# Kernel optimization log

Measured on AMD Instinct MI355X. Metric: run time of the kernel, lower is better.

## Reference

```python
import jax, jax.numpy as jnp
import numpy as np

MASK_ID = -100
L, D, HID, NH = 10, 768, 3072, 12
DH = D // NH
REACH = 2  # (sliding_window_size - 1) // 2 with window 5


def _layernorm(x, g, b, eps=1e-5):
    mu = x.mean(-1, keepdims=True)
    var = ((x - mu) ** 2).mean(-1, keepdims=True)
    return (x - mu) * jax.lax.rsqrt(var + eps) * g + b


def _adaln(x, temb, w, bb, g, be):
    # AdaLayerNormShiftScale: linear(silu(temb)) -> (scale, shift)
    e = jax.nn.silu(temb) @ w + bb
    scale, shift = jnp.split(e, 2, axis=-1)
    return _layernorm(x, g, be) * (1.0 + scale) + shift


def _timestep_emb(t):
    half = D // 2
    exponent = -np.log(10000.0) * jnp.arange(half, dtype=jnp.float32) / (half - 1.0)
    freq = jnp.exp(exponent)  # [half]
    emb = t.astype(jnp.float32)[..., None] * freq  # [b,s,half]
    return jnp.concatenate([jnp.sin(emb), jnp.cos(emb)], axis=-1)  # [b,s,D]


def setup_inputs():
    key = jax.random.key(0)
    ks = jax.random.split(key, 16)
    b, s = 4, 1024
    # packed token ids: 4 samples of 256 tokens (16x16 grid), last 64 tokens padding
    idx = np.arange(s)
    sid = idx // 256
    hpos = (idx % 256) // 16
    wpos = idx % 16
    sid = np.where(idx >= 960, MASK_ID, sid)
    tok = np.stack([sid, hpos, wpos], axis=-1)  # [s,3]
    token_ids = jnp.asarray(np.broadcast_to(tok, (b, s, 3)).copy(), dtype=jnp.int32)
    t = jax.random.randint(ks[0], (b, 1), 0, L + 1).astype(jnp.int32)
    t = jnp.broadcast_to(t, (b, s))

    def w(k, shape):
        return jax.random.normal(k, shape, jnp.float32) * 0.02

    return dict(
        x=jax.random.normal(ks[1], (b, s, D), jnp.float32),
        t=t,
        token_ids=token_ids,
        proj_in_w=w(ks[2], (D, D)), proj_in_b=jnp.zeros((D,), jnp.float32),
        h_emb=w(ks[3], (64, D)), w_emb=w(ks[4], (64, D)),
        adaln1_w=w(ks[5], (L, D, 2 * D)), adaln1_b=jnp.zeros((L, 2 * D), jnp.float32),
        ln1_g=jnp.ones((L, D), jnp.float32), ln1_b=jnp.zeros((L, D), jnp.float32),
        qkv_w=w(ks[6], (L, D, 3 * D)), qkv_b=jnp.zeros((L, 3 * D), jnp.float32),
        o_w=w(ks[7], (L, D, D)), o_b=jnp.zeros((L, D), jnp.float32),
        adaln2_w=w(ks[8], (L, D, 2 * D)), adaln2_b=jnp.zeros((L, 2 * D), jnp.float32),
        ln2_g=jnp.ones((L, D), jnp.float32), ln2_b=jnp.zeros((L, D), jnp.float32),
        fc1_w=w(ks[9], (L, D, HID)), fc1_b=jnp.zeros((L, HID), jnp.float32),
        fc2_w=w(ks[10], (L, HID, D)), fc2_b=jnp.zeros((L, D), jnp.float32),
        nout_w=w(ks[11], (D, 2 * D)), nout_b=jnp.zeros((2 * D,), jnp.float32),
        nout_g=jnp.ones((D,), jnp.float32), nout_beta=jnp.zeros((D,), jnp.float32),
    )


def _encoder(x, t, token_ids, proj_in_w, proj_in_b, h_emb, w_emb,
             adaln1_w, adaln1_b, ln1_g, ln1_b, qkv_w, qkv_b, o_w, o_b,
             adaln2_w, adaln2_b, ln2_g, ln2_b, fc1_w, fc1_b, fc2_w, fc2_b,
             nout_w, nout_b, nout_g, nout_beta):
    b, s, _ = x.shape
    sample_ids = token_ids[..., 0]          # [b,s]
    pos = token_ids[..., 1:]                # [b,s,2]
    x = x @ proj_in_w + proj_in_b
    x = x + h_emb[pos[..., 0]] + w_emb[pos[..., 1]]

    # block-sparse mask: same packed sample, Chebyshev sliding window, no padding queries
    same = sample_ids[:, :, None] == sample_ids[:, None, :]              # [b,s,s]
    cheby = jnp.abs(pos[:, :, None, :] - pos[:, None, :, :]).max(-1)      # [b,s,s]
    notpad_q = (sample_ids != MASK_ID)[:, :, None]
    mask = same & (cheby <= REACH) & notpad_q                             # [b,s,s]
    row_valid = mask.any(-1)[..., None]                                   # [b,s,1]

    temb = _timestep_emb(t)  # [b,s,D]
    scale = 1.0 / np.sqrt(DH)
    for i in range(L):
        h1 = _adaln(x, temb, adaln1_w[i], adaln1_b[i], ln1_g[i], ln1_b[i])
        qkv = h1 @ qkv_w[i] + qkv_b[i]
        q, k, v = jnp.split(qkv, 3, axis=-1)
        q = q.reshape(b, s, NH, DH)
        k = k.reshape(b, s, NH, DH)
        v = v.reshape(b, s, NH, DH)
        scores = jnp.einsum('bqhd,bkhd->bhqk', q, k) * scale
        scores = jnp.where(mask[:, None], scores, -1e30)
        attn = jax.nn.softmax(scores, axis=-1)
        o = jnp.einsum('bhqk,bkhd->bqhd', attn, v).reshape(b, s, D)
        o = jnp.where(row_valid, o, 0.0)  # fully-masked (padding) rows -> 0
        x = x + o @ o_w[i] + o_b[i]
        h2 = _adaln(x, temb, adaln2_w[i], adaln2_b[i], ln2_g[i], ln2_b[i])
        x = x + jax.nn.gelu(h2 @ fc1_w[i] + fc1_b[i], approximate=False) @ fc2_w[i] + fc2_b[i]
    x = _adaln(x, temb, nout_w, nout_b, nout_g, nout_beta)
    return x


def reference(x, t, token_ids, proj_in_w, proj_in_b, h_emb, w_emb,
              adaln1_w, adaln1_b, ln1_g, ln1_b, qkv_w, qkv_b, o_w, o_b,
              adaln2_w, adaln2_b, ln2_g, ln2_b, fc1_w, fc1_b, fc2_w, fc2_b,
              nout_w, nout_b, nout_g, nout_beta):
    return _encoder(x, t, token_ids, proj_in_w, proj_in_b, h_emb, w_emb,
                    adaln1_w, adaln1_b, ln1_g, ln1_b, qkv_w, qkv_b, o_w, o_b,
                    adaln2_w, adaln2_b, ln2_g, ln2_b, fc1_w, fc1_b, fc2_w, fc2_b,
                    nout_w, nout_b, nout_g, nout_beta)
```

## Files before the change

### kernel.cpp

```cpp
#include <hip/hip_runtime.h>
#include <hip/hip_bf16.h>
#include <math.h>

#define MASK_ID (-100)
#define SEQ 1024
#define BATCH 4
#define DMODEL 768
#define NHEAD 12
#define DHEAD 64
#define NLAYER 10
#define HIDDEN 3072

typedef unsigned short ushort_t;
typedef unsigned int uint_t;

__device__ __forceinline__ ushort_t f2bf(float f) {
    uint_t u = __float_as_uint(f);
    u = u + 0x7fffu + ((u >> 16) & 1u);
    return (ushort_t)(u >> 16);
}
__device__ __forceinline__ float bf2f(ushort_t u) {
    return __uint_as_float(((uint_t)u) << 16);
}

__device__ __forceinline__ void async_ld16(ushort_t* lds, const ushort_t* g) {
    __builtin_amdgcn_global_load_lds((__attribute__((address_space(1))) const void*)g,
                                     (__attribute__((address_space(3))) void*)lds, 16, 0, 0);
}

__global__ void temb_silu_kernel(const int* __restrict__ t, float* __restrict__ stemb) {
    int b = blockIdx.x;
    int j = threadIdx.x;
    float tv = (float)t[b * SEQ];
    float freq = expf(-logf(10000.f) * (float)j / 383.f);
    float arg = tv * freq;
    float s = sinf(arg), c = cosf(arg);
    stemb[b * DMODEL + j]       = s / (1.f + expf(-s));
    stemb[b * DMODEL + 384 + j] = c / (1.f + expf(-c));
}

__global__ __launch_bounds__(256)
void adaln_partial_kernel(const float* __restrict__ stemb,
                          const float* __restrict__ a1w,
                          const float* __restrict__ a2w,
                          const float* __restrict__ nw,
                          float* __restrict__ partial) {
    int chunk = blockIdx.x;
    int kc    = blockIdx.y;
    int slot  = blockIdx.z;
    int tid = threadIdx.x;
    int col = chunk * 256 + tid;
    const float* W;
    if (slot == 20) W = nw;
    else {
        int i = slot >> 1;
        W = ((slot & 1) ? a2w : a1w) + (size_t)i * DMODEL * 2 * DMODEL;
    }
    __shared__ float sb[4 * 96];
    for (int idx = tid; idx < 4 * 96; idx += 256) {
        int bb = idx / 96, kk = idx % 96;
        sb[idx] = stemb[bb * DMODEL + kc * 96 + kk];
    }
    __syncthreads();
    const float* Wp = W + (size_t)(kc * 96) * (2 * DMODEL) + col;
    float a0 = 0.f, a1 = 0.f, a2 = 0.f, a3 = 0.f;
    #pragma unroll 4
    for (int kk = 0; kk < 96; ++kk) {
        float w = Wp[(size_t)kk * (2 * DMODEL)];
        a0 = fmaf(sb[kk], w, a0);
        a1 = fmaf(sb[96 + kk], w, a1);
        a2 = fmaf(sb[192 + kk], w, a2);
        a3 = fmaf(sb[288 + kk], w, a3);
    }
    size_t base = ((size_t)(slot * 8 + kc) * 4) * (2 * DMODEL) + col;
    partial[base + 0 * 2 * DMODEL] = a0;
    partial[base + 1 * 2 * DMODEL] = a1;
    partial[base + 2 * 2 * DMODEL] = a2;
    partial[base + 3 * 2 * DMODEL] = a3;
}

__global__ __launch_bounds__(256)
void adaln_reduce_kernel(const float* __restrict__ partial,
                         const float* __restrict__ a1b, const float* __restrict__ a2b,
                         const float* __restrict__ nb,
                         float* __restrict__ e_all) {
    int chunk = blockIdx.x;
    int slot  = blockIdx.y;
    int col = chunk * 256 + threadIdx.x;
    const float* bb;
    if (slot == 20) bb = nb;
    else {
        int i = slot >> 1;
        bb = ((slot & 1) ? a2b : a1b) + i * 2 * DMODEL;
    }
    float bias = bb[col];
    float s0 = bias, s1 = bias, s2 = bias, s3 = bias;
    #pragma unroll
    for (int kc = 0; kc < 8; ++kc) {
        size_t base = ((size_t)(slot * 8 + kc) * 4) * (2 * DMODEL) + col;
        s0 += partial[base + 0 * 2 * DMODEL];
        s1 += partial[base + 1 * 2 * DMODEL];
        s2 += partial[base + 2 * 2 * DMODEL];
        s3 += partial[base + 3 * 2 * DMODEL];
    }
    size_t o = (size_t)slot * 4 * (2 * DMODEL) + col;
    e_all[o + 0 * 2 * DMODEL] = s0;
    e_all[o + 1 * 2 * DMODEL] = s1;
    e_all[o + 2 * 2 * DMODEL] = s2;
    e_all[o + 3 * 2 * DMODEL] = s3;
}

__global__ __launch_bounds__(256)
void transpose_bf16_kernel(const float* __restrict__ in, ushort_t* __restrict__ out,
                           int R, int C) {
    __shared__ float tile[32][33];
    int tx = threadIdx.x & 31, ty = threadIdx.x >> 5;
    int c0 = blockIdx.x * 32, r0 = blockIdx.y * 32;
    #pragma unroll
    for (int i = 0; i < 4; ++i)
        tile[ty + 8 * i][tx] = in[(size_t)(r0 + ty + 8 * i) * C + c0 + tx];
    __syncthreads();
    #pragma unroll
    for (int i = 0; i < 4; ++i)
        out[(size_t)(c0 + ty + 8 * i) * R + r0 + tx] = f2bf(tile[tx][ty + 8 * i]);
}

__global__ __launch_bounds__(256)
void transpose_all_kernel(const float* __restrict__ w0, const float* __restrict__ w1,
                          const float* __restrict__ w2, const float* __restrict__ w3,
                          ushort_t* __restrict__ o0, ushort_t* __restrict__ o1,
                          ushort_t* __restrict__ o2, ushort_t* __restrict__ o3) {
    int layer = blockIdx.y;
    int id = blockIdx.x;
    const float* in; ushort_t* out; int R, C, tile_id, TX;
    if (id < 1728) {
        in = w0 + (size_t)layer * DMODEL * 3 * DMODEL; out = o0 + (size_t)layer * 3 * DMODEL * DMODEL;
        R = DMODEL; C = 3 * DMODEL; tile_id = id; TX = 72;
    } else if (id < 2304) {
        in = w1 + (size_t)layer * DMODEL * DMODEL; out = o1 + (size_t)layer * DMODEL * DMODEL;
        R = DMODEL; C = DMODEL; tile_id = id - 1728; TX = 24;
    } else if (id < 4608) {
        in = w2 + (size_t)layer * DMODEL * HIDDEN; out = o2 + (size_t)layer * HIDDEN * DMODEL;
        R = DMODEL; C = HIDDEN; tile_id = id - 2304; TX = 96;
    } else {
        in = w3 + (size_t)layer * HIDDEN * DMODEL; out = o3 + (size_t)layer * DMODEL * HIDDEN;
        R = HIDDEN; C = DMODEL; tile_id = id - 4608; TX = 24;
    }
    int c0 = (tile_id % TX) * 32, r0 = (tile_id / TX) * 32;
    __shared__ float tile[32][33];
    int tx = threadIdx.x & 31, ty = threadIdx.x >> 5;
    #pragma unroll
    for (int i = 0; i < 4; ++i)
        tile[ty + 8 * i][tx] = in[(size_t)(r0 + ty + 8 * i) * C + c0 + tx];
    __syncthreads();
    #pragma unroll
    for (int i = 0; i < 4; ++i)
        out[(size_t)(c0 + ty + 8 * i) * R + r0 + tx] = f2bf(tile[tx][ty + 8 * i]);
}

__global__ __launch_bounds__(256)
void f32_to_bf16_kernel(const float* __restrict__ in, ushort_t* __restrict__ out, int n8) {
    int i = blockIdx.x * 256 + threadIdx.x;
    if (i >= n8) return;
    float4 a = ((const float4*)in)[2 * i];
    float4 b = ((const float4*)in)[2 * i + 1];
    uint4 o;
    o.x = (uint_t)f2bf(a.x) | ((uint_t)f2bf(a.y) << 16);
    o.y = (uint_t)f2bf(a.z) | ((uint_t)f2bf(a.w) << 16);
    o.z = (uint_t)f2bf(b.x) | ((uint_t)f2bf(b.y) << 16);
    o.w = (uint_t)f2bf(b.z) | ((uint_t)f2bf(b.w) << 16);
    ((uint4*)out)[i] = o;
}

template<int OUT_BF>
__global__ __launch_bounds__(256)
void ln_adaln_kernel(const float* __restrict__ in, void* __restrict__ outv,
                     const float* __restrict__ g, const float* __restrict__ be,
                     const float* __restrict__ e) {
    int row = blockIdx.x;
    int b = row >> 10;
    const float* xr = in + (size_t)row * DMODEL;
    int tid = threadIdx.x;
    float v0 = xr[tid], v1 = xr[tid + 256], v2 = xr[tid + 512];
    float s = v0 + v1 + v2;
    float ss = v0 * v0 + v1 * v1 + v2 * v2;
    #pragma unroll
    for (int o = 32; o; o >>= 1) { s += __shfl_down(s, o); ss += __shfl_down(ss, o); }
    __shared__ float ls[4], lss[4];
    __shared__ float mu_s, rs_s;
    int wid = tid >> 6, lane = tid & 63;
    if (lane == 0) { ls[wid] = s; lss[wid] = ss; }
    __syncthreads();
    if (tid == 0) {
        float S = ls[0] + ls[1] + ls[2] + ls[3];
        float SS = lss[0] + lss[1] + lss[2] + lss[3];
        float mu = S * (1.f / DMODEL);
        float var = SS * (1.f / DMODEL) - mu * mu;
        mu_s = mu;
        rs_s = rsqrtf(var + 1e-5f);
    }
    __syncthreads();
    float mu = mu_s, rs = rs_s;
    const float* esc = e + (size_t)b * (2 * DMODEL);
    #pragma unroll
    for (int j = 0; j < 3; ++j) {
        int c = tid + j * 256;
        float v = (j == 0) ? v0 : (j == 1) ? v1 : v2;
        float y = (v - mu) * rs * g[c] + be[c];
        y = y * (1.f + esc[c]) + esc[DMODEL + c];
        if (OUT_BF) ((ushort_t*)outv)[(size_t)row * DMODEL + c] = f2bf(y);
        else        ((float*)outv)[(size_t)row * DMODEL + c] = y;
    }
}

__device__ __forceinline__ float gelu_exact(float x) {
    return 0.5f * x * (1.f + erff(x * 0.70710678118654752f));
}

template<int BM, int BN, int EPI>
__global__ __launch_bounds__(256, 2)
void gemm_bf16(const ushort_t* __restrict__ A, const ushort_t* __restrict__ Wt,
               const float* __restrict__ bias, void* __restrict__ outv,
               const float* __restrict__ emb_h, const float* __restrict__ emb_w,
               const int* __restrict__ tok,
               int M, int N, int K) {
    constexpr int WM = BM / 2, WN = BN / 2;
    constexpr int FM = WM / 16, FN = WN / 16;
    constexpr int HALF = (BM + BN) * 64;
    using f32x4  = __attribute__((ext_vector_type(4))) float;
    using bf16x8 = __attribute__((ext_vector_type(8))) short;

    __shared__ __align__(16) ushort_t lds[2 * HALF];

    int tid = threadIdx.x;
    int lane = tid & 63, wid = tid >> 6;
    int wr = wid >> 1, wc = wid & 1;
    int l16 = lane & 15, lg = lane >> 4;

    int nx = N / BN;
    int cpx = gridDim.x >> 3;
    int wg = blockIdx.x;
    int wgid = (wg & 7) * cpx + (wg >> 3);
    int bx = wgid % nx, by = wgid / nx;
    int bm0 = by * BM, bn0 = bx * BN;

    f32x4 acc[FM][FN];
    #pragma unroll
    for (int m = 0; m < FM; ++m)
        #pragma unroll
        for (int n = 0; n < FN; ++n)
            #pragma unroll
            for (int r = 0; r < 4; ++r) acc[m][n][r] = 0.f;

    const ushort_t* Abase = A + (size_t)bm0 * K;
    const ushort_t* Bbase = Wt + (size_t)bn0 * K;

    #define STAGE(bufoff, kt)                                                        \
        do {                                                                         \
            _Pragma("unroll")                                                        \
            for (int s2 = 0; s2 < BM / 32; ++s2) {                                   \
                int ca = s2 * 256 + tid;                                             \
                async_ld16(&lds[(bufoff) + ca * 8],                                  \
                           Abase + (size_t)(ca >> 3) * K + (kt) * 64 + (ca & 7) * 8);\
            }                                                                        \
            _Pragma("unroll")                                                        \
            for (int s2 = 0; s2 < BN / 32; ++s2) {                                   \
                int ca = s2 * 256 + tid;                                             \
                async_ld16(&lds[(bufoff) + BM * 64 + ca * 8],                        \
                           Bbase + (size_t)(ca >> 3) * K + (kt) * 64 + (ca & 7) * 8);\
            }                                                                        \
        } while (0)

    int nk = K >> 6;
    STAGE(0, 0);
    int curoff = 0;
    for (int kt = 0; kt < nk; ++kt) {
        asm volatile("s_waitcnt vmcnt(0)" ::: "memory");
        __syncthreads();
        if (kt + 1 < nk) STAGE(curoff ^ HALF, kt + 1);
        #pragma unroll
        for (int kk = 0; kk < 2; ++kk) {
            bf16x8 af[FM], bfr[FN];
            #pragma unroll
            for (int m = 0; m < FM; ++m)
                af[m] = *(const bf16x8*)&lds[curoff + (wr * WM + m * 16 + l16) * 64 + kk * 32 + lg * 8];
            #pragma unroll
            for (int n = 0; n < FN; ++n)
                bfr[n] = *(const bf16x8*)&lds[curoff + BM * 64 + (wc * WN + n * 16 + l16) * 64 + kk * 32 + lg * 8];
            #pragma unroll
            for (int m = 0; m < FM; ++m)
                #pragma unroll
                for (int n = 0; n < FN; ++n)
                    acc[m][n] = __builtin_amdgcn_mfma_f32_16x16x32_bf16(af[m], bfr[n], acc[m][n], 0, 0, 0);
        }
        curoff ^= HALF;
    }
    #undef STAGE

    int r0 = bm0 + wr * WM, c0 = bn0 + wc * WN;
    #pragma unroll
    for (int m = 0; m < FM; ++m) {
        #pragma unroll
        for (int n = 0; n < FN; ++n) {
            int cc = c0 + n * 16 + l16;
            float bcol = bias[cc];
            #pragma unroll
            for (int r = 0; r < 4; ++r) {
                int row = r0 + m * 16 + lg * 4 + r;
                float v = acc[m][n][r] + bcol;
                if (EPI == 0) {
                    ((ushort_t*)outv)[(size_t)row * N + cc] = f2bf(v);
                } else if (EPI == 1) {
                    int p0 = tok[row * 3 + 1], p1 = tok[row * 3 + 2];
                    v += emb_h[p0 * DMODEL + cc] + emb_w[p1 * DMODEL + cc];
                    ((float*)outv)[(size_t)row * N + cc] = v;
                } else if (EPI == 2) {
                    float* op = (float*)outv + (size_t)row * N + cc;
                    *op = *op + v;
                } else {
                    ((ushort_t*)outv)[(size_t)row * N + cc] = f2bf(gelu_exact(v));
                }
            }
        }
    }
}

__global__ __launch_bounds__(256)
void attn_kernel(const ushort_t* __restrict__ qkv, const int* __restrict__ tok,
                 ushort_t* __restrict__ o_out) {
    int tid = threadIdx.x;
    int u = tid >> 2, part = tid & 3;
    int q = blockIdx.x * 16 + (u & 15);
    int h = blockIdx.y * 4 + (u >> 4);
    int b = blockIdx.z;
    int m = b * SEQ + q;
    ushort_t* op = o_out + (size_t)m * DMODEL + h * DHEAD + part * 16;
    int sid = tok[m * 3];
    if (sid == MASK_ID) {
        uint4 z = {0u, 0u, 0u, 0u};
        ((uint4*)op)[0] = z;
        ((uint4*)op)[1] = z;
        return;
    }
    int qh = tok[m * 3 + 1], qw = tok[m * 3 + 2];
    const ushort_t* qp = qkv + (size_t)m * (3 * DMODEL) + h * DHEAD + part * 16;
    float qv[16], ov[16];
    {
        uint4 u0 = ((const uint4*)qp)[0];
        uint4 u1 = ((const uint4*)qp)[1];
        qv[0] = bf2f(u0.x & 0xffff); qv[1] = bf2f(u0.x >> 16);
        qv[2] = bf2f(u0.y & 0xffff); qv[3] = bf2f(u0.y >> 16);
        qv[4] = bf2f(u0.z & 0xffff); qv[5] = bf2f(u0.z >> 16);
        qv[6] = bf2f(u0.w & 0xffff); qv[7] = bf2f(u0.w >> 16);
        qv[8]  = bf2f(u1.x & 0xffff); qv[9]  = bf2f(u1.x >> 16);
        qv[10] = bf2f(u1.y & 0xffff); qv[11] = bf2f(u1.y >> 16);
        qv[12] = bf2f(u1.z & 0xffff); qv[13] = bf2f(u1.z >> 16);
        qv[14] = bf2f(u1.w & 0xffff); qv[15] = bf2f(u1.w >> 16);
    }
    #pragma unroll
    for (int i = 0; i < 16; ++i) ov[i] = 0.f;
    float mx = -1e30f, den = 0.f;
    for (int dh = -2; dh <= 2; ++dh) {
        for (int dw = -2; dw <= 2; ++dw) {
            int kq = q + dh * 16 + dw;
            if (kq < 0 || kq >= SEQ) continue;
            int km = b * SEQ + kq;
            if (tok[km * 3] != sid) continue;
            int kh2 = tok[km * 3 + 1], kw2 = tok[km * 3 + 2];
            int adh = kh2 - qh; if (adh < 0) adh = -adh;
            int adw = kw2 - qw; if (adw < 0) adw = -adw;
            if (adh > 2 || adw > 2) continue;
            const ushort_t* kp = qkv + (size_t)km * (3 * DMODEL) + DMODEL + h * DHEAD + part * 16;
            float dot;
            {
                uint4 u0 = ((const uint4*)kp)[0];
                uint4 u1 = ((const uint4*)kp)[1];
                dot = qv[0] * bf2f(u0.x & 0xffff);
                dot = fmaf(qv[1], bf2f(u0.x >> 16), dot);
                dot = fmaf(qv[2], bf2f(u0.y & 0xffff), dot);
                dot = fmaf(qv[3], bf2f(u0.y >> 16), dot);
                dot = fmaf(qv[4], bf2f(u0.z & 0xffff), dot);
                dot = fmaf(qv[5], bf2f(u0.z >> 16), dot);
                dot = fmaf(qv[6], bf2f(u0.w & 0xffff), dot);
                dot = fmaf(qv[7], bf2f(u0.w >> 16), dot);
                dot = fmaf(qv[8],  bf2f(u1.x & 0xffff), dot);
                dot = fmaf(qv[9],  bf2f(u1.x >> 16), dot);
                dot = fmaf(qv[10], bf2f(u1.y & 0xffff), dot);
                dot = fmaf(qv[11], bf2f(u1.y >> 16), dot);
                dot = fmaf(qv[12], bf2f(u1.z & 0xffff), dot);
                dot = fmaf(qv[13], bf2f(u1.z >> 16), dot);
                dot = fmaf(qv[14], bf2f(u1.w & 0xffff), dot);
                dot = fmaf(qv[15], bf2f(u1.w >> 16), dot);
            }
            dot += __shfl_xor(dot, 1);
            dot += __shfl_xor(dot, 2);
            float sc = dot * 0.125f;
            float nm = fmaxf(mx, sc);
            float c1 = expf(mx - nm);
            float c2 = expf(sc - nm);
            den = den * c1 + c2;
            const ushort_t* vp = qkv + (size_t)km * (3 * DMODEL) + 2 * DMODEL + h * DHEAD + part * 16;
            {
                uint4 u0 = ((const uint4*)vp)[0];
                uint4 u1 = ((const uint4*)vp)[1];
                ov[0] = ov[0] * c1 + c2 * bf2f(u0.x & 0xffff);
                ov[1] = ov[1] * c1 + c2 * bf2f(u0.x >> 16);
                ov[2] = ov[2] * c1 + c2 * bf2f(u0.y & 0xffff);
                ov[3] = ov[3] * c1 + c2 * bf2f(u0.y >> 16);
                ov[4] = ov[4] * c1 + c2 * bf2f(u0.z & 0xffff);
                ov[5] = ov[5] * c1 + c2 * bf2f(u0.z >> 16);
                ov[6] = ov[6] * c1 + c2 * bf2f(u0.w & 0xffff);
                ov[7] = ov[7] * c1 + c2 * bf2f(u0.w >> 16);
                ov[8]  = ov[8]  * c1 + c2 * bf2f(u1.x & 0xffff);
                ov[9]  = ov[9]  * c1 + c2 * bf2f(u1.x >> 16);
                ov[10] = ov[10] * c1 + c2 * bf2f(u1.y & 0xffff);
                ov[11] = ov[11] * c1 + c2 * bf2f(u1.y >> 16);
                ov[12] = ov[12] * c1 + c2 * bf2f(u1.z & 0xffff);
                ov[13] = ov[13] * c1 + c2 * bf2f(u1.z >> 16);
                ov[14] = ov[14] * c1 + c2 * bf2f(u1.w & 0xffff);
                ov[15] = ov[15] * c1 + c2 * bf2f(u1.w >> 16);
            }
            mx = nm;
        }
    }
    float inv = 1.f / den;
    uint4 o0, o1;
    o0.x = (uint_t)f2bf(ov[0] * inv) | ((uint_t)f2bf(ov[1] * inv) << 16);
    o0.y = (uint_t)f2bf(ov[2] * inv) | ((uint_t)f2bf(ov[3] * inv) << 16);
    o0.z = (uint_t)f2bf(ov[4] * inv) | ((uint_t)f2bf(ov[5] * inv) << 16);
    o0.w = (uint_t)f2bf(ov[6] * inv) | ((uint_t)f2bf(ov[7] * inv) << 16);
    o1.x = (uint_t)f2bf(ov[8]  * inv) | ((uint_t)f2bf(ov[9]  * inv) << 16);
    o1.y = (uint_t)f2bf(ov[10] * inv) | ((uint_t)f2bf(ov[11] * inv) << 16);
    o1.z = (uint_t)f2bf(ov[12] * inv) | ((uint_t)f2bf(ov[13] * inv) << 16);
    o1.w = (uint_t)f2bf(ov[14] * inv) | ((uint_t)f2bf(ov[15] * inv) << 16);
    ((uint4*)op)[0] = o0;
    ((uint4*)op)[1] = o1;
}

extern "C" void kernel_launch(void* const* d_in, const int* in_sizes, int n_in,
                              void* d_out, int out_size, void* d_ws, size_t ws_size,
                              hipStream_t stream) {
    const float* x_in      = (const float*)d_in[0];
    const int*   t         = (const int*)d_in[1];
    const int*   tok       = (const int*)d_in[2];
    const float* proj_in_w = (const float*)d_in[3];
    const float* proj_in_b = (const float*)d_in[4];
    const float* h_emb     = (const float*)d_in[5];
    const float* w_emb     = (const float*)d_in[6];
    const float* adaln1_w  = (const float*)d_in[7];
    const float* adaln1_b  = (const float*)d_in[8];
    const float* ln1_g     = (const float*)d_in[9];
    const float* ln1_b     = (const float*)d_in[10];
    const float* qkv_w     = (const float*)d_in[11];
    const float* qkv_b     = (const float*)d_in[12];
    const float* o_w       = (const float*)d_in[13];
    const float* o_b       = (const float*)d_in[14];
    const float* adaln2_w  = (const float*)d_in[15];
    const float* adaln2_b  = (const float*)d_in[16];
    const float* ln2_g     = (const float*)d_in[17];
    const float* ln2_b     = (const float*)d_in[18];
    const float* fc1_w     = (const float*)d_in[19];
    const float* fc1_b     = (const float*)d_in[20];
    const float* fc2_w     = (const float*)d_in[21];
    const float* fc2_b     = (const float*)d_in[22];
    const float* nout_w    = (const float*)d_in[23];
    const float* nout_b    = (const float*)d_in[24];
    const float* nout_g    = (const float*)d_in[25];
    const float* nout_beta = (const float*)d_in[26];

    const int M = BATCH * SEQ;

    float* stemb   = (float*)d_ws;
    float* e_all   = stemb + BATCH * DMODEL;
    float* partial = e_all + 21 * BATCH * 2 * DMODEL;
    ushort_t* h_bf   = (ushort_t*)(partial + 21 * 8 * 4 * 2 * DMODEL);
    ushort_t* qkv_bf = h_bf + (size_t)M * DMODEL;
    ushort_t* hid_bf = qkv_bf + (size_t)M * 3 * DMODEL;
    ushort_t* projT  = hid_bf + (size_t)M * HIDDEN;
    ushort_t* qkvT_a = projT + (size_t)DMODEL * DMODEL;
    ushort_t* oT_a   = qkvT_a + (size_t)NLAYER * 3 * DMODEL * DMODEL;
    ushort_t* fc1T_a = oT_a + (size_t)NLAYER * DMODEL * DMODEL;
    ushort_t* fc2T_a = fc1T_a + (size_t)NLAYER * DMODEL * HIDDEN;
    float* x = (float*)d_out;

    temb_silu_kernel<<<BATCH, 384, 0, stream>>>(t, stemb);
    adaln_partial_kernel<<<dim3(6, 8, 2 * NLAYER + 1), 256, 0, stream>>>(
        stemb, adaln1_w, adaln2_w, nout_w, partial);
    adaln_reduce_kernel<<<dim3(6, 2 * NLAYER + 1), 256, 0, stream>>>(
        partial, adaln1_b, adaln2_b, nout_b, e_all);

    transpose_all_kernel<<<dim3(6912, NLAYER), 256, 0, stream>>>(
        qkv_w, o_w, fc1_w, fc2_w, qkvT_a, oT_a, fc1T_a, fc2T_a);
    transpose_bf16_kernel<<<dim3(DMODEL / 32, DMODEL / 32), 256, 0, stream>>>(proj_in_w, projT, DMODEL, DMODEL);

    f32_to_bf16_kernel<<<(M * DMODEL / 8 + 255) / 256, 256, 0, stream>>>(x_in, h_bf, M * DMODEL / 8);
    gemm_bf16<64, 64, 1><<<(DMODEL / 64) * (M / 64), 256, 0, stream>>>(
        h_bf, projT, proj_in_b, x, h_emb, w_emb, tok, M, DMODEL, DMODEL);

    for (int i = 0; i < NLAYER; ++i) {
        ln_adaln_kernel<1><<<M, 256, 0, stream>>>(
            x, h_bf, ln1_g + i * DMODEL, ln1_b + i * DMODEL,
            e_all + (size_t)(2 * i) * BATCH * 2 * DMODEL);
        gemm_bf16<128, 128, 0><<<(3 * DMODEL / 128) * (M / 128), 256, 0, stream>>>(
            h_bf, qkvT_a + (size_t)i * 3 * DMODEL * DMODEL, qkv_b + i * 3 * DMODEL,
            qkv_bf, nullptr, nullptr, nullptr, M, 3 * DMODEL, DMODEL);
        attn_kernel<<<dim3(SEQ / 16, NHEAD / 4, BATCH), 256, 0, stream>>>(qkv_bf, tok, h_bf);
        gemm_bf16<64, 64, 2><<<(DMODEL / 64) * (M / 64), 256, 0, stream>>>(
            h_bf, oT_a + (size_t)i * DMODEL * DMODEL, o_b + i * DMODEL,
            x, nullptr, nullptr, nullptr, M, DMODEL, DMODEL);
        ln_adaln_kernel<1><<<M, 256, 0, stream>>>(
            x, h_bf, ln2_g + i * DMODEL, ln2_b + i * DMODEL,
            e_all + (size_t)(2 * i + 1) * BATCH * 2 * DMODEL);
        gemm_bf16<128, 128, 3><<<(HIDDEN / 128) * (M / 128), 256, 0, stream>>>(
            h_bf, fc1T_a + (size_t)i * DMODEL * HIDDEN, fc1_b + i * HIDDEN,
            hid_bf, nullptr, nullptr, nullptr, M, HIDDEN, DMODEL);
        gemm_bf16<64, 64, 2><<<(DMODEL / 64) * (M / 64), 256, 0, stream>>>(
            hid_bf, fc2T_a + (size_t)i * DMODEL * HIDDEN, fc2_b + i * DMODEL,
            x, nullptr, nullptr, nullptr, M, DMODEL, HIDDEN);
    }

    ln_adaln_kernel<0><<<M, 256, 0, stream>>>(
        x, x, nout_g, nout_beta, e_all + (size_t)(2 * NLAYER) * BATCH * 2 * DMODEL);
}
```

Measured before the change: 1.914 ms.

## Triple-buffer GEMM LDS with XOR swizzle and retile QKV/FC1 to 64x128

Moves the bf16 GEMM from double to triple buffering, issuing loads two k-tiles ahead and waiting only on the older tile's vmcnt. This is meant to hide global-load latency behind the MFMA work. An XOR swizzle on the LDS column chunk removes bank conflicts on fragment reads, and s_setprio raises wave priority during the MFMA section. The QKV and FC1 GEMMs switch from 128x128 to 64x128 tiles, which doubles the block count for better CU occupancy. The cost is more LDS per block, and the hardcoded vmcnt thresholds must match the load count per thread.

```diff
diff --git a/kernel.cpp b/kernel.cpp
--- a/kernel.cpp
+++ b/kernel.cpp
@@ -27,6 +27,8 @@
     __builtin_amdgcn_global_load_lds((__attribute__((address_space(1))) const void*)g,
                                      (__attribute__((address_space(3))) void*)lds, 16, 0, 0);
 }
+
+#define WAITVM(n) asm volatile("s_waitcnt vmcnt(" #n ")" ::: "memory")
 
 __global__ void temb_silu_kernel(const int* __restrict__ t, float* __restrict__ stemb) {
     int b = blockIdx.x;
@@ -226,16 +228,18 @@
                int M, int N, int K) {
     constexpr int WM = BM / 2, WN = BN / 2;
     constexpr int FM = WM / 16, FN = WN / 16;
-    constexpr int HALF = (BM + BN) * 64;
+    constexpr int BUF = (BM + BN) * 64;
+    constexpr int LPT = (BM + BN) / 32;
     using f32x4  = __attribute__((ext_vector_type(4))) float;
     using bf16x8 = __attribute__((ext_vector_type(8))) short;
 
-    __shared__ __align__(16) ushort_t lds[2 * HALF];
+    __shared__ __align__(16) ushort_t lds[3 * BUF];
 
     int tid = threadIdx.x;
     int lane = tid & 63, wid = tid >> 6;
     int wr = wid >> 1, wc = wid & 1;
     int l16 = lane & 15, lg = lane >> 4;
+    int sw = l16 & 7;
 
     int nx = N / BN;
     int cpx = gridDim.x >> 3;
@@ -255,45 +259,64 @@
     const ushort_t* Abase = A + (size_t)bm0 * K;
     const ushort_t* Bbase = Wt + (size_t)bn0 * K;
 
-    #define STAGE(bufoff, kt)                                                        \
-        do {                                                                         \
-            _Pragma("unroll")                                                        \
-            for (int s2 = 0; s2 < BM / 32; ++s2) {                                   \
-                int ca = s2 * 256 + tid;                                             \
-                async_ld16(&lds[(bufoff) + ca * 8],                                  \
-                           Abase + (size_t)(ca >> 3) * K + (kt) * 64 + (ca & 7) * 8);\
-            }                                                                        \
-            _Pragma("unroll")                                                        \
-            for (int s2 = 0; s2 < BN / 32; ++s2) {                                   \
-                int ca = s2 * 256 + tid;                                             \
-                async_ld16(&lds[(bufoff) + BM * 64 + ca * 8],                        \
-                           Bbase + (size_t)(ca >> 3) * K + (kt) * 64 + (ca & 7) * 8);\
-            }                                                                        \
+    #define STAGE(bufi, kt)                                                             \
+        do {                                                                            \
+            _Pragma("unroll")                                                           \
+            for (int s2 = 0; s2 < BM / 32; ++s2) {                                      \
+                int ca = s2 * 256 + tid;                                                \
+                int rw = ca >> 3, kcs = (ca & 7) ^ (rw & 7);                            \
+                async_ld16(&lds[(bufi) * BUF + ca * 8],                                 \
+                           Abase + (size_t)rw * K + (kt) * 64 + kcs * 8);               \
+            }                                                                           \
+            _Pragma("unroll")                                                           \
+            for (int s2 = 0; s2 < BN / 32; ++s2) {                                      \
+                int ca = s2 * 256 + tid;                                                \
+                int rw = ca >> 3, kcs = (ca & 7) ^ (rw & 7);                            \
+                async_ld16(&lds[(bufi) * BUF + BM * 64 + ca * 8],                       \
+                           Bbase + (size_t)rw * K + (kt) * 64 + kcs * 8);               \
+            }                                                                           \
         } while (0)
 
     int nk = K >> 6;
     STAGE(0, 0);
-    int curoff = 0;
+    STAGE(1, 1);
+    int bufi = 0;
     for (int kt = 0; kt < nk; ++kt) {
-        asm volatile("s_waitcnt vmcnt(0)" ::: "memory");
-        __syncthreads();
-        if (kt + 1 < nk) STAGE(curoff ^ HALF, kt + 1);
+        int nxt = bufi + 2; if (nxt >= 3) nxt -= 3;
+        if (kt + 2 < nk) {
+            STAGE(nxt, kt + 2);
+            if constexpr (LPT == 4) WAITVM(8); else WAITVM(12);
+        } else if (kt + 1 < nk) {
+            if constexpr (LPT == 4) WAITVM(4); else WAITVM(6);
+        } else {
+            WAITVM(0);
+        }
+        __builtin_amdgcn_s_barrier();
+        __builtin_amdgcn_s_setprio(1);
         #pragma unroll
         for (int kk = 0; kk < 2; ++kk) {
             bf16x8 af[FM], bfr[FN];
             #pragma unroll
-            for (int m = 0; m < FM; ++m)
-                af[m] = *(const bf16x8*)&lds[curoff + (wr * WM + m * 16 + l16) * 64 + kk * 32 + lg * 8];
+            for (int m = 0; m < FM; ++m) {
+                int row = wr * WM + m * 16 + l16;
+                int csw = (kk * 4 + lg) ^ sw;
+                af[m] = *(const bf16x8*)&lds[bufi * BUF + row * 64 + csw * 8];
+            }
             #pragma unroll
-            for (int n = 0; n < FN; ++n)
-                bfr[n] = *(const bf16x8*)&lds[curoff + BM * 64 + (wc * WN + n * 16 + l16) * 64 + kk * 32 + lg * 8];
+            for (int n = 0; n < FN; ++n) {
+                int row = wc * WN + n * 16 + l16;
+                int csw = (kk * 4 + lg) ^ sw;
+                bfr[n] = *(const bf16x8*)&lds[bufi * BUF + BM * 64 + row * 64 + csw * 8];
+            }
             #pragma unroll
             for (int m = 0; m < FM; ++m)
                 #pragma unroll
                 for (int n = 0; n < FN; ++n)
                     acc[m][n] = __builtin_amdgcn_mfma_f32_16x16x32_bf16(af[m], bfr[n], acc[m][n], 0, 0, 0);
         }
-        curoff ^= HALF;
+        __builtin_amdgcn_s_setprio(0);
+        __builtin_amdgcn_s_barrier();
+        ++bufi; if (bufi >= 3) bufi = 0;
     }
     #undef STAGE
 
@@ -501,7 +524,7 @@
         ln_adaln_kernel<1><<<M, 256, 0, stream>>>(
             x, h_bf, ln1_g + i * DMODEL, ln1_b + i * DMODEL,
             e_all + (size_t)(2 * i) * BATCH * 2 * DMODEL);
-        gemm_bf16<128, 128, 0><<<(3 * DMODEL / 128) * (M / 128), 256, 0, stream>>>(
+        gemm_bf16<64, 128, 0><<<(3 * DMODEL / 128) * (M / 64), 256, 0, stream>>>(
             h_bf, qkvT_a + (size_t)i * 3 * DMODEL * DMODEL, qkv_b + i * 3 * DMODEL,
             qkv_bf, nullptr, nullptr, nullptr, M, 3 * DMODEL, DMODEL);
         attn_kernel<<<dim3(SEQ / 16, NHEAD / 4, BATCH), 256, 0, stream>>>(qkv_bf, tok, h_bf);
@@ -511,7 +534,7 @@
         ln_adaln_kernel<1><<<M, 256, 0, stream>>>(
             x, h_bf, ln2_g + i * DMODEL, ln2_b + i * DMODEL,
             e_all + (size_t)(2 * i + 1) * BATCH * 2 * DMODEL);
-        gemm_bf16<128, 128, 3><<<(HIDDEN / 128) * (M / 128), 256, 0, stream>>>(
+        gemm_bf16<64, 128, 3><<<(HIDDEN / 128) * (M / 64), 256, 0, stream>>>(
             h_bf, fc1T_a + (size_t)i * DMODEL * HIDDEN, fc1_b + i * HIDDEN,
             hid_bf, nullptr, nullptr, nullptr, M, HIDDEN, DMODEL);
         gemm_bf16<64, 64, 2><<<(DMODEL / 64) * (M / 64), 256, 0, stream>>>(
```

Result: faster. 1.847 ms (-3.5%).
